# Performance work log

Measured on AMD Instinct MI355X. Metric: run time of the kernel, lower is better.

Reference implementation:

```python
import jax, jax.numpy as jnp
import numpy as np

B, D, T, NT, DS, G = 1024, 512, 36, 64, 32, 4
EPS = 1e-5


def setup_inputs() -> dict:
    key = jax.random.key(0)
    ks = jax.random.split(key, 8)
    return {
        "x": jax.random.normal(ks[0], (B, D, T, 1), jnp.float32),
        "y": jax.random.normal(ks[1], (B, D, T, 1), jnp.float32),
        "my_tokens": jax.random.normal(ks[2], (NT, D), jnp.float32) * 0.02,
        "gate": jax.random.normal(ks[3], (1,), jnp.float32) * 0.1,
        "gate_av": jax.random.normal(ks[4], (1,), jnp.float32) * 0.1,
        "w_down": jax.random.normal(ks[5], (DS, D // G), jnp.float32) * 0.05,  # Conv2d(512->32,1,groups=4) weight [32,128,1,1] squeezed
        "w_up": jax.random.normal(ks[6], (D, DS // G), jnp.float32) * 0.05,    # Conv2d(32->512,1,groups=4) weight [512,8,1,1] squeezed
        "bn1_g": jnp.ones((DS,), jnp.float32), "bn1_b": jnp.zeros((DS,), jnp.float32),
        "bn2_g": jnp.ones((D,), jnp.float32), "bn2_b": jnp.zeros((D,), jnp.float32),
        "lnb_g": jnp.ones((D,), jnp.float32), "lnb_b": jnp.zeros((D,), jnp.float32),
        "lnp_g": jnp.ones((D,), jnp.float32), "lnp_b": jnp.zeros((D,), jnp.float32),
    }


def _layernorm(h, g, b):  # normalize last dim
    mu = jnp.mean(h, axis=-1, keepdims=True)
    var = jnp.var(h, axis=-1, keepdims=True)
    return (h - mu) * jax.lax.rsqrt(var + EPS) * g + b


def _batchnorm(z, g, b):  # z: [B,C,T], training-mode batch stats over (B,T)
    mu = jnp.mean(z, axis=(0, 2), keepdims=True)
    var = jnp.var(z, axis=(0, 2), keepdims=True)
    return (z - mu) * jax.lax.rsqrt(var + EPS) * g[None, :, None] + b[None, :, None]


def reference(x, y, my_tokens, gate, gate_av, w_down, w_up,
              bn1_g, bn1_b, bn2_g, bn2_b, lnb_g, lnb_b, lnp_g, lnp_b):
    xs = x[..., 0]  # [B,D,T]
    ys = y[..., 0]  # [B,D,T]
    # token <- y cross attention
    att_y2tk = jax.nn.softmax(jnp.einsum('td,bds->bts', my_tokens, ys), axis=-1)  # [B,NT,T]
    rep = my_tokens[None] + jnp.einsum('bts,bds->btd', att_y2tk, ys)  # [B,NT,D]
    # x <- token cross attention
    att_tk2x = jax.nn.softmax(jnp.einsum('bds,btd->bst', xs, rep), axis=-1)  # [B,T,NT]
    x_res = jnp.einsum('bst,btd->bsd', att_tk2x, rep)  # [B,T,D]
    xc = xs + gate_av[0] * jnp.swapaxes(x_res, 1, 2)  # [B,D,T]
    # ln_before over channel dim
    h = jnp.swapaxes(_layernorm(jnp.swapaxes(xc, 1, 2), lnb_g, lnb_b), 1, 2)  # [B,D,T]
    # grouped 1x1 down conv
    hg = h.reshape(h.shape[0], G, D // G, T)
    z = jnp.einsum('bgct,goc->bgot', hg, w_down.reshape(G, DS // G, D // G)).reshape(h.shape[0], DS, T)
    z = jax.nn.relu(_batchnorm(z, bn1_g, bn1_b))
    # grouped 1x1 up conv
    zg = z.reshape(z.shape[0], G, DS // G, T)
    o = jnp.einsum('bgct,goc->bgot', zg, w_up.reshape(G, D // G, DS // G)).reshape(z.shape[0], D, T)
    o = _batchnorm(o, bn2_g, bn2_b)
    o = jnp.swapaxes(_layernorm(jnp.swapaxes(o, 1, 2), lnp_g, lnp_b), 1, 2)
    return (gate[0] * o)[..., None]  # [B,D,T,1]
```

## Files before the change

### kernel.cpp

```cpp
#include <hip/hip_runtime.h>

#define B_ 1024
#define D_ 512
#define T_ 36
#define NT_ 64
#define DS_ 32
#define EPS_ 1e-5f

typedef float f32x4 __attribute__((ext_vector_type(4)));
typedef __bf16 bf16x8 __attribute__((ext_vector_type(8)));
typedef unsigned short u16x8 __attribute__((ext_vector_type(8)));
typedef unsigned short u16x4 __attribute__((ext_vector_type(4)));

#define DEVI static __device__ __forceinline__
#define MFMA16 __builtin_amdgcn_mfma_f32_16x16x32_bf16

DEVI unsigned short f2bf(float f) { return __builtin_bit_cast(unsigned short, (__bf16)f); }
DEVI float bf2f(unsigned short h) { return (float)__builtin_bit_cast(__bf16, h); }

DEVI unsigned swz(int row, int col) {
    return (unsigned)(row * 1024 + ((2 * col) ^ ((row & 7) << 4)));
}

DEVI f32x4 tile16_gl(const unsigned short* __restrict__ Arow, const char* img, int brow, int l4)
{
    f32x4 acc0 = {0.f,0.f,0.f,0.f}, acc1 = {0.f,0.f,0.f,0.f};
    #pragma unroll
    for (int ks = 0; ks < 16; ks += 2) {
        int ka = ks * 32 + l4 * 8, kb = ka + 32;
        acc0 = MFMA16(*(const bf16x8*)(Arow + ka), *(const bf16x8*)(img + swz(brow, ka)), acc0, 0, 0, 0);
        acc1 = MFMA16(*(const bf16x8*)(Arow + kb), *(const bf16x8*)(img + swz(brow, kb)), acc1, 0, 0, 0);
    }
    return acc0 + acc1;
}

DEVI f32x4 tile16_ll(const char* imgA, int arow, const char* imgB, int brow, int l4)
{
    f32x4 acc0 = {0.f,0.f,0.f,0.f}, acc1 = {0.f,0.f,0.f,0.f};
    #pragma unroll
    for (int ks = 0; ks < 16; ks += 2) {
        int ka = ks * 32 + l4 * 8, kb = ka + 32;
        acc0 = MFMA16(*(const bf16x8*)(imgA + swz(arow, ka)), *(const bf16x8*)(imgB + swz(brow, ka)), acc0, 0, 0, 0);
        acc1 = MFMA16(*(const bf16x8*)(imgA + swz(arow, kb)), *(const bf16x8*)(imgB + swz(brow, kb)), acc1, 0, 0, 0);
    }
    return acc0 + acc1;
}

#define OFF_XST 49152
#define OFF_SC  98304
#define OFF_A1  109056
#define OFF_A1T 118272
#define OFF_A2  125184
#define OFF_GT  132096
#define OFF_W   139008
#define K1_LDS  145920

__global__ __launch_bounds__(512)
void k0_prepack(const float* __restrict__ tok, const float* __restrict__ wd,
                unsigned short* __restrict__ tokbf, unsigned short* __restrict__ tokT,
                unsigned short* __restrict__ wdd)
{
    int i = blockIdx.x * 512 + threadIdx.x;
    if (i < 32768) {
        tokbf[i] = f2bf(tok[i]);
    } else if (i < 65536) {
        int j = i - 32768; int d = j >> 6, t = j & 63;
        tokT[j] = f2bf(tok[t * 512 + d]);
    } else if (i < 81920) {
        int j = i - 65536; int o = j >> 9, dd = j & 511;
        wdd[j] = ((dd >> 7) == (o >> 3)) ? f2bf(wd[o * 128 + (dd & 127)]) : (unsigned short)0;
    }
}

DEVI void stage_unit(const float* __restrict__ src, char* __restrict__ dst, int u)
{
    int dblk = u / 9, s4 = u - dblk * 9;
    int s0 = s4 * 4;
    const float* bp = src + dblk * 8 * T_ + s0;
    u16x8 u0, u1, u2, u3;
    #pragma unroll
    for (int r = 0; r < 8; ++r) {
        f32x4 v = *(const f32x4*)(bp + r * T_);
        u0[r] = f2bf(v[0]); u1[r] = f2bf(v[1]);
        u2[r] = f2bf(v[2]); u3[r] = f2bf(v[3]);
    }
    *(u16x8*)(dst + swz(s0 + 0, dblk * 8)) = u0;
    *(u16x8*)(dst + swz(s0 + 1, dblk * 8)) = u1;
    *(u16x8*)(dst + swz(s0 + 2, dblk * 8)) = u2;
    *(u16x8*)(dst + swz(s0 + 3, dblk * 8)) = u3;
}

__global__ __launch_bounds__(1024, 4)
void k1_fused(const float* __restrict__ x, const float* __restrict__ y,
              const unsigned short* __restrict__ tokbf, const unsigned short* __restrict__ tokT,
              const float* __restrict__ gav_p, const unsigned short* __restrict__ wdd,
              const float* __restrict__ lnbg, const float* __restrict__ lnbb,
              float* __restrict__ z_pre)
{
    extern __shared__ char lds[];
    float* sc = (float*)(lds + OFF_SC);
    unsigned short* a1  = (unsigned short*)(lds + OFF_A1);
    unsigned short* a1t = (unsigned short*)(lds + OFF_A1T);
    unsigned short* a2  = (unsigned short*)(lds + OFF_A2);
    unsigned short* gt  = (unsigned short*)(lds + OFF_GT);
    unsigned short* wb  = (unsigned short*)(lds + OFF_W);

    const int b    = blockIdx.x;
    const int tid  = threadIdx.x;
    const int lane = tid & 63;
    const int w    = tid >> 6;
    const int l15  = lane & 15;
    const int l4   = lane >> 4;

    const float* yb = y + b * (D_ * T_);
    const float* xb = x + b * (D_ * T_);

    if (tid < 576) {
        stage_unit(yb, lds, tid);
    } else {
        int z = tid - 576;
        unsigned* z1 = (unsigned*)(lds + 36 * 1024);
        for (int i = z; i < 3072; i += 448) z1[i] = 0u;
        unsigned* z2 = (unsigned*)(lds + OFF_XST + 36 * 1024);
        for (int i = z; i < 3072; i += 448) z2[i] = 0u;
        unsigned* z3 = (unsigned*)(lds + OFF_A1);
        for (int i = z; i < 9216; i += 448) z3[i] = 0u;
    }
    __syncthreads();

    if (w < 12) {
        int mt = w / 3, nt = w % 3;
        int trow = mt * 16 + l15, srow = nt * 16 + l15;
        f32x4 acc = tile16_gl(tokbf + trow * 512, lds, srow, l4);
        if (srow < T_) {
            #pragma unroll
            for (int j = 0; j < 4; ++j)
                sc[(mt * 16 + l4 * 4 + j) * 42 + srow] = acc[j];
        }
    } else {
        for (int u = tid - 768; u < 576; u += 256)
            stage_unit(xb, lds + OFF_XST, u);
    }
    __syncthreads();

    if (w < 9) {
        int mt = w / 3, nt = w % 3;
        int arow = mt * 16 + l15, brow = nt * 16 + l15;
        f32x4 acc = tile16_ll(lds + OFF_XST, arow, lds, brow, l4);
        #pragma unroll
        for (int j = 0; j < 4; ++j) {
            int gr = mt * 16 + l4 * 4 + j;
            if (gr < T_) gt[gr * 72 + brow] = f2bf(acc[j]);
        }
    }
    __syncthreads();

    {
        int t = tid >> 4, l16 = tid & 15;
        const float* scp = sc + t * 42;
        float v0 = scp[l16];
        float v1 = scp[l16 + 16];
        float v2 = (l16 < 4) ? scp[l16 + 32] : -1e30f;
        float m = fmaxf(fmaxf(v0, v1), v2);
        #pragma unroll
        for (int off = 1; off < 16; off <<= 1) m = fmaxf(m, __shfl_xor(m, off));
        float e0 = __expf(v0 - m), e1 = __expf(v1 - m);
        float e2 = (l16 < 4) ? __expf(v2 - m) : 0.f;
        float ssum = e0 + e1 + e2;
        #pragma unroll
        for (int off = 1; off < 16; off <<= 1) ssum += __shfl_xor(ssum, off);
        float inv = 1.f / ssum;
        unsigned short h0 = f2bf(e0 * inv), h1 = f2bf(e1 * inv);
        a1[t * 72 + l16] = h0;       a1[t * 72 + l16 + 16] = h1;
        a1t[l16 * 72 + t] = h0;      a1t[(l16 + 16) * 72 + t] = h1;
        if (l16 < 4) {
            unsigned short h2 = f2bf(e2 * inv);
            a1[t * 72 + l16 + 32] = h2;
            a1t[(l16 + 32) * 72 + t] = h2;
        }
    }
    f32x4 py0[2], py1[2], py2[2];
    #pragma unroll
    for (int mi = 0; mi < 2; ++mi) {
        const float* yrow = yb + ((2 * w + mi) * 16 + l15) * T_;
        py0[mi] = *(const f32x4*)(yrow + l4 * 8);
        py1[mi] = *(const f32x4*)(yrow + l4 * 8 + 4);
        if (l4 == 0) py2[mi] = *(const f32x4*)(yrow + 32);
        else         py2[mi] = (f32x4){0.f, 0.f, 0.f, 0.f};
    }
    __syncthreads();

    if (w < 12) {
        int mt = w / 3, nt = w % 3;
        int trow = mt * 16 + l15, srow = nt * 16 + l15;
        bf16x8 sa0 = *(const bf16x8*)(a1 + trow * 72 + l4 * 8);
        bf16x8 sa1 = *(const bf16x8*)(a1 + trow * 72 + 32 + l4 * 8);
        bf16x8 sb0 = *(const bf16x8*)(gt + srow * 72 + l4 * 8);
        bf16x8 sb1 = *(const bf16x8*)(gt + srow * 72 + 32 + l4 * 8);
        f32x4 acc = tile16_gl(tokbf + trow * 512, lds + OFF_XST, srow, l4);
        acc = MFMA16(sa0, sb0, acc, 0, 0, 0);
        acc = MFMA16(sa1, sb1, acc, 0, 0, 0);
        if (srow < T_) {
            #pragma unroll
            for (int j = 0; j < 4; ++j)
                sc[(mt * 16 + l4 * 4 + j) * 42 + srow] = acc[j];
        }
    }
    __syncthreads();

    if (tid < 768) {
        int s = tid >> 4, l16 = tid & 15;
        if (s < T_) {
            float v0 = sc[(l16) * 42 + s];
            float v1 = sc[(l16 + 16) * 42 + s];
            float v2 = sc[(l16 + 32) * 42 + s];
            float v3 = sc[(l16 + 48) * 42 + s];
            float m = fmaxf(fmaxf(v0, v1), fmaxf(v2, v3));
            #pragma unroll
            for (int off = 1; off < 16; off <<= 1) m = fmaxf(m, __shfl_xor(m, off));
            float e0 = __expf(v0 - m), e1 = __expf(v1 - m), e2 = __expf(v2 - m), e3 = __expf(v3 - m);
            float ssum = e0 + e1 + e2 + e3;
            #pragma unroll
            for (int off = 1; off < 16; off <<= 1) ssum += __shfl_xor(ssum, off);
            float inv = 1.f / ssum;
            a2[s * 72 + l16]      = f2bf(e0 * inv);
            a2[s * 72 + l16 + 16] = f2bf(e1 * inv);
            a2[s * 72 + l16 + 32] = f2bf(e2 * inv);
            a2[s * 72 + l16 + 48] = f2bf(e3 * inv);
        }
    }
    __syncthreads();

    if (w < 9) {
        int mt = w / 3, nt = w % 3;
        f32x4 acc = {0.f, 0.f, 0.f, 0.f};
        #pragma unroll
        for (int ks = 0; ks < 2; ++ks) {
            int k0 = ks * 32 + l4 * 8;
            acc = MFMA16(*(const bf16x8*)(a2 + (mt * 16 + l15) * 72 + k0),
                         *(const bf16x8*)(a1t + (nt * 16 + l15) * 72 + k0), acc, 0, 0, 0);
        }
        #pragma unroll
        for (int j = 0; j < 4; ++j)
            wb[(mt * 16 + l4 * 4 + j) * 72 + nt * 16 + l15] = f2bf(acc[j]);
    }
    __syncthreads();

    {
        const float gav = gav_p[0];
        f32x4 acc[2][3];
        #pragma unroll
        for (int mi = 0; mi < 2; ++mi)
            #pragma unroll
            for (int n = 0; n < 3; ++n) acc[mi][n] = (f32x4){0.f, 0.f, 0.f, 0.f};

        bf16x8 aT[2][2], aY[2][2];
        #pragma unroll
        for (int mi = 0; mi < 2; ++mi) {
            int d = (2 * w + mi) * 16 + l15;
            aT[mi][0] = *(const bf16x8*)(tokT + d * 64 + l4 * 8);
            aT[mi][1] = *(const bf16x8*)(tokT + d * 64 + 32 + l4 * 8);
            bf16x8 t0, t1;
            #pragma unroll
            for (int j = 0; j < 4; ++j) {
                t0[j] = (__bf16)py0[mi][j]; t0[4 + j] = (__bf16)py1[mi][j];
                t1[j] = (__bf16)py2[mi][j]; t1[4 + j] = (__bf16)0.f;
            }
            aY[mi][0] = t0; aY[mi][1] = t1;
        }
        #pragma unroll
        for (int n = 0; n < 3; ++n) {
            int srow = n * 16 + l15;
            bf16x8 b20 = *(const bf16x8*)(a2 + srow * 72 + l4 * 8);
            bf16x8 b21 = *(const bf16x8*)(a2 + srow * 72 + 32 + l4 * 8);
            bf16x8 bw0 = *(const bf16x8*)(wb + srow * 72 + l4 * 8);
            bf16x8 bw1 = *(const bf16x8*)(wb + srow * 72 + 32 + l4 * 8);
            #pragma unroll
            for (int mi = 0; mi < 2; ++mi) {
                acc[mi][n] = MFMA16(aT[mi][0], b20, acc[mi][n], 0, 0, 0);
                acc[mi][n] = MFMA16(aT[mi][1], b21, acc[mi][n], 0, 0, 0);
                acc[mi][n] = MFMA16(aY[mi][0], bw0, acc[mi][n], 0, 0, 0);
                acc[mi][n] = MFMA16(aY[mi][1], bw1, acc[mi][n], 0, 0, 0);
            }
        }

        float* red = sc;
        float rs_[3] = {0.f, 0.f, 0.f}, rq_[3] = {0.f, 0.f, 0.f};
        #pragma unroll
        for (int mi = 0; mi < 2; ++mi) {
            int dcol = (2 * w + mi) * 16 + l4 * 4;
            #pragma unroll
            for (int n = 0; n < 3; ++n) {
                int s = n * 16 + l15;
                if (s < T_) {
                    u16x4 xv = *(const u16x4*)(lds + OFF_XST + swz(s, dcol));
                    #pragma unroll
                    for (int j = 0; j < 4; ++j) {
                        float v = bf2f(xv[j]) + gav * acc[mi][n][j];
                        acc[mi][n][j] = v;
                        rs_[n] += v; rq_[n] += v * v;
                    }
                }
            }
        }
        #pragma unroll
        for (int n = 0; n < 3; ++n) {
            rs_[n] += __shfl_xor(rs_[n], 16); rq_[n] += __shfl_xor(rq_[n], 16);
            rs_[n] += __shfl_xor(rs_[n], 32); rq_[n] += __shfl_xor(rq_[n], 32);
        }
        if (l4 == 0) {
            #pragma unroll
            for (int n = 0; n < 3; ++n) {
                int s = n * 16 + l15;
                if (s < T_) { red[s * 16 + w] = rs_[n]; red[768 + s * 16 + w] = rq_[n]; }
            }
        }
        __syncthreads();
        if (tid < T_) {
            int s = tid; float S = 0.f, Q = 0.f;
            #pragma unroll
            for (int q = 0; q < 16; ++q) { S += red[s * 16 + q]; Q += red[768 + s * 16 + q]; }
            float mu = S * (1.f / 512.f);
            float var = Q * (1.f / 512.f) - mu * mu;
            red[1536 + s] = mu; red[1584 + s] = rsqrtf(var + EPS_);
        }
        __syncthreads();

        #pragma unroll
        for (int mi = 0; mi < 2; ++mi) {
            int dcol = (2 * w + mi) * 16 + l4 * 4;
            f32x4 gv  = *(const f32x4*)(lnbg + dcol);
            f32x4 bv2 = *(const f32x4*)(lnbb + dcol);
            #pragma unroll
            for (int n = 0; n < 3; ++n) {
                int s = n * 16 + l15;
                if (s < T_) {
                    float mu = red[1536 + s], rsg = red[1584 + s];
                    u16x4 hv;
                    #pragma unroll
                    for (int j = 0; j < 4; ++j)
                        hv[j] = f2bf((acc[mi][n][j] - mu) * rsg * gv[j] + bv2[j]);
                    *(u16x4*)(lds + swz(s, dcol)) = hv;
                }
            }
        }
    }
    __syncthreads();

    if (w < 6) {
        int mt = w / 3, nt = w % 3;
        int orow = mt * 16 + l15, srow = nt * 16 + l15;
        f32x4 acc = tile16_gl(wdd + orow * 512, lds, srow, l4);
        if (srow < T_) {
            #pragma unroll
            for (int j = 0; j < 4; ++j)
                z_pre[b * (DS_ * T_) + (mt * 16 + l4 * 4 + j) * T_ + srow] = acc[j];
        }
    }
}

__global__ __launch_bounds__(256)
void k3_bn1(const float* __restrict__ z_pre, float* __restrict__ st1)
{
    __shared__ float rbuf[4][2];
    int o = blockIdx.x;
    int tid = threadIdx.x;
    float S = 0.f, Q = 0.f;
    for (int i = tid; i < B_ * T_; i += 256) {
        int b = i / T_, t = i - b * T_;
        float v = z_pre[b * (DS_ * T_) + o * T_ + t];
        S += v; Q += v * v;
    }
    #pragma unroll
    for (int off = 1; off < 64; off <<= 1) { S += __shfl_xor(S, off); Q += __shfl_xor(Q, off); }
    int ww = tid >> 6;
    if ((tid & 63) == 0) { rbuf[ww][0] = S; rbuf[ww][1] = Q; }
    __syncthreads();
    if (tid == 0) {
        float s2 = 0.f, q2 = 0.f;
        for (int i = 0; i < 4; ++i) { s2 += rbuf[i][0]; q2 += rbuf[i][1]; }
        float mu = s2 / 36864.f;
        float var = q2 / 36864.f - mu * mu;
        st1[o] = mu; st1[32 + o] = rsqrtf(var + EPS_);
    }
}

__global__ __launch_bounds__(256)
void k4m_moments(const float* __restrict__ z_pre, const float* __restrict__ st1,
                 const float* __restrict__ g1p, const float* __restrict__ b1p,
                 float* __restrict__ m4)
{
    __shared__ float zr[32][40];
    int blk = blockIdx.x, tid = threadIdx.x;
    int c2 = tid & 7, c1 = (tid >> 3) & 7, g = tid >> 6;
    int ch1 = g * 8 + c1, ch2 = g * 8 + c2;
    float acc = 0.f, asum = 0.f;
    for (int bi = 0; bi < 8; ++bi) {
        int b = blk * 8 + bi;
        __syncthreads();
        for (int i = tid; i < DS_ * T_; i += 256) {
            int o = i / T_, t = i - o * T_;
            float v = z_pre[b * (DS_ * T_) + i];
            zr[o][t] = fmaxf(0.f, (v - st1[o]) * st1[32 + o] * g1p[o] + b1p[o]);
        }
        __syncthreads();
        for (int t = 0; t < T_; ++t) {
            float a = zr[ch1][t], b2 = zr[ch2][t];
            acc += a * b2;
            asum += a;
        }
    }
    m4[blk * 288 + tid] = acc;
    if (c1 == c2) m4[blk * 288 + 256 + g * 8 + c1] = asum;
}

__global__ __launch_bounds__(512)
void k4s_bn2stats(const float* __restrict__ m4, const float* __restrict__ wu,
                  float* __restrict__ st2)
{
    __shared__ float M2[256], mz[32];
    int tid = threadIdx.x;
    if (tid < 256) {
        float S = 0.f;
        for (int k = 0; k < 128; ++k) S += m4[k * 288 + tid];
        M2[tid] = S * (1.f / 36864.f);
    } else if (tid < 288) {
        int j = tid - 256;
        float S = 0.f;
        for (int k = 0; k < 128; ++k) S += m4[k * 288 + 256 + j];
        mz[j] = S * (1.f / 36864.f);
    }
    __syncthreads();
    int d = tid, g = d >> 7;
    float wr[8];
    #pragma unroll
    for (int c = 0; c < 8; ++c) wr[c] = wu[d * 8 + c];
    float mu2 = 0.f;
    #pragma unroll
    for (int c = 0; c < 8; ++c) mu2 += wr[c] * mz[g * 8 + c];
    float e2 = 0.f;
    #pragma unroll
    for (int c = 0; c < 8; ++c)
        #pragma unroll
        for (int c2 = 0; c2 < 8; ++c2)
            e2 += wr[c] * wr[c2] * M2[g * 64 + c * 8 + c2];
    st2[d] = mu2;
    st2[512 + d] = rsqrtf(e2 - mu2 * mu2 + EPS_);
}

#define K5_LDS 47888
__global__ __launch_bounds__(512, 6)
void k5_final(const float* __restrict__ z_pre, const float* __restrict__ st1,
              const float* __restrict__ g1p, const float* __restrict__ b1p,
              const float* __restrict__ wu, const float* __restrict__ st2,
              const float* __restrict__ g2p, const float* __restrict__ b2p,
              const float* __restrict__ lnpg, const float* __restrict__ lnpb,
              const float* __restrict__ gate_p, float* __restrict__ out)
{
    extern __shared__ char lds[];
    unsigned short* o_f = (unsigned short*)lds;
    float* zrT = (float*)(lds + 41984);
    int b = blockIdx.x;
    int tid = threadIdx.x;

    for (int i = tid; i < DS_ * T_; i += 512) {
        int o = i / T_, s = i - o * T_;
        float v = z_pre[b * (DS_ * T_) + i];
        zrT[s * 41 + o] = fmaxf(0.f, (v - st1[o]) * st1[32 + o] * g1p[o] + b1p[o]);
    }
    __syncthreads();

    for (int i = tid; i < D_ * T_; i += 512) {
        int d = i / T_, t = i - d * T_;
        const float* zp = &zrT[t * 41 + (d >> 7) * 8];
        const float* wp = &wu[d * 8];
        f32x4 w0 = *(const f32x4*)wp;
        f32x4 w1 = *(const f32x4*)(wp + 4);
        float acc = zp[0]*w0[0] + zp[1]*w0[1] + zp[2]*w0[2] + zp[3]*w0[3]
                  + zp[4]*w1[0] + zp[5]*w1[1] + zp[6]*w1[2] + zp[7]*w1[3];
        o_f[d * 41 + t] = f2bf((acc - st2[d]) * st2[512 + d] * g2p[d] + b2p[d]);
    }
    __syncthreads();

    int w = tid >> 6, lane = tid & 63;
    float gate = gate_p[0];
    for (int t = w; t < T_; t += 8) {
        float S = 0.f, Q = 0.f;
        float v[8];
        #pragma unroll
        for (int i2 = 0; i2 < 8; ++i2) {
            float vv = bf2f(o_f[(i2 * 64 + lane) * 41 + t]);
            v[i2] = vv; S += vv; Q += vv * vv;
        }
        #pragma unroll
        for (int off = 1; off < 64; off <<= 1) { S += __shfl_xor(S, off); Q += __shfl_xor(Q, off); }
        float mu = S * (1.f / 512.f);
        float var = Q * (1.f / 512.f) - mu * mu;
        float rs = rsqrtf(var + EPS_);
        #pragma unroll
        for (int i2 = 0; i2 < 8; ++i2) {
            int d = i2 * 64 + lane;
            o_f[d * 41 + t] = f2bf(gate * ((v[i2] - mu) * rs * lnpg[d] + lnpb[d]));
        }
    }
    __syncthreads();

    float* ob = out + b * (D_ * T_);
    for (int i = tid; i < D_ * T_; i += 512) {
        int d = i / T_, t = i - d * T_;
        ob[i] = bf2f(o_f[d * 41 + t]);
    }
}

extern "C" void kernel_launch(void* const* d_in, const int* in_sizes, int n_in,
                              void* d_out, int out_size, void* d_ws, size_t ws_size,
                              hipStream_t stream)
{
    (void)in_sizes; (void)n_in; (void)out_size; (void)ws_size;
    const float* x    = (const float*)d_in[0];
    const float* y    = (const float*)d_in[1];
    const float* tok  = (const float*)d_in[2];
    const float* gate = (const float*)d_in[3];
    const float* gav  = (const float*)d_in[4];
    const float* wd   = (const float*)d_in[5];
    const float* wu   = (const float*)d_in[6];
    const float* bn1g = (const float*)d_in[7];
    const float* bn1b = (const float*)d_in[8];
    const float* bn2g = (const float*)d_in[9];
    const float* bn2b = (const float*)d_in[10];
    const float* lnbg = (const float*)d_in[11];
    const float* lnbb = (const float*)d_in[12];
    const float* lnpg = (const float*)d_in[13];
    const float* lnpb = (const float*)d_in[14];
    float* out = (float*)d_out;

    char* ws = (char*)d_ws;
    float* z_pre          = (float*)ws;
    float* st1            = (float*)(ws + 4718592);
    unsigned short* tokbf = (unsigned short*)(ws + 4719104);
    unsigned short* tokT  = (unsigned short*)(ws + 4784640);
    unsigned short* wdd   = (unsigned short*)(ws + 4850176);
    float* m4             = (float*)(ws + 4882944);
    float* st2            = (float*)(ws + 5030400);

    hipFuncSetAttribute((const void*)k1_fused, hipFuncAttributeMaxDynamicSharedMemorySize, K1_LDS);
    hipFuncSetAttribute((const void*)k5_final, hipFuncAttributeMaxDynamicSharedMemorySize, K5_LDS);

    k0_prepack<<<160, 512, 0, stream>>>(tok, wd, tokbf, tokT, wdd);
    k1_fused<<<B_, 1024, K1_LDS, stream>>>(x, y, tokbf, tokT, gav, wdd, lnbg, lnbb, z_pre);
    k3_bn1<<<DS_, 256, 0, stream>>>(z_pre, st1);
    k4m_moments<<<128, 256, 0, stream>>>(z_pre, st1, bn1g, bn1b, m4);
    k4s_bn2stats<<<1, 512, 0, stream>>>(m4, wu, st2);
    k5_final<<<B_, 512, K5_LDS, stream>>>(z_pre, st1, bn1g, bn1b, wu, st2, bn2g, bn2b,
                                          lnpg, lnpb, gate, out);
}
```

Before: 224.7 us.

## Split BN1 stats into 512-block partial reduction and move softmax to idle waves

The BN1 statistics kernel previously ran only 32 blocks, each striding over all 1024 batches. It is now split into a 512-block partial-sum pass and a small final reduction, so many more CUs share the reduction. In k1_fused, the first softmax moves off its own barrier phase onto waves 12-15, which were idle during the score GEMM, with each thread handling 9 elements. This removes one __syncthreads and overlaps the softmax with the tile GEMM, at the cost of one extra kernel launch and a workspace layout shift.

```diff
diff --git a/kernel.cpp b/kernel.cpp
--- a/kernel.cpp
+++ b/kernel.cpp
@@ -152,31 +152,27 @@
             int gr = mt * 16 + l4 * 4 + j;
             if (gr < T_) gt[gr * 72 + brow] = f2bf(acc[j]);
         }
-    }
-    __syncthreads();
-
-    {
-        int t = tid >> 4, l16 = tid & 15;
-        const float* scp = sc + t * 42;
-        float v0 = scp[l16];
-        float v1 = scp[l16 + 16];
-        float v2 = (l16 < 4) ? scp[l16 + 32] : -1e30f;
-        float m = fmaxf(fmaxf(v0, v1), v2);
-        #pragma unroll
-        for (int off = 1; off < 16; off <<= 1) m = fmaxf(m, __shfl_xor(m, off));
-        float e0 = __expf(v0 - m), e1 = __expf(v1 - m);
-        float e2 = (l16 < 4) ? __expf(v2 - m) : 0.f;
-        float ssum = e0 + e1 + e2;
-        #pragma unroll
-        for (int off = 1; off < 16; off <<= 1) ssum += __shfl_xor(ssum, off);
+    } else if (w >= 12) {
+        int t = (tid - 768) >> 2, l2 = tid & 3;
+        const float* scp = sc + t * 42 + l2 * 9;
+        float v[9];
+        float m = -1e30f;
+        #pragma unroll
+        for (int j = 0; j < 9; ++j) { v[j] = scp[j]; m = fmaxf(m, v[j]); }
+        m = fmaxf(m, __shfl_xor(m, 1));
+        m = fmaxf(m, __shfl_xor(m, 2));
+        float e[9], ssum = 0.f;
+        #pragma unroll
+        for (int j = 0; j < 9; ++j) { e[j] = __expf(v[j] - m); ssum += e[j]; }
+        ssum += __shfl_xor(ssum, 1);
+        ssum += __shfl_xor(ssum, 2);
         float inv = 1.f / ssum;
-        unsigned short h0 = f2bf(e0 * inv), h1 = f2bf(e1 * inv);
-        a1[t * 72 + l16] = h0;       a1[t * 72 + l16 + 16] = h1;
-        a1t[l16 * 72 + t] = h0;      a1t[(l16 + 16) * 72 + t] = h1;
-        if (l16 < 4) {
-            unsigned short h2 = f2bf(e2 * inv);
-            a1[t * 72 + l16 + 32] = h2;
-            a1t[(l16 + 32) * 72 + t] = h2;
+        #pragma unroll
+        for (int j = 0; j < 9; ++j) {
+            unsigned short h = f2bf(e[j] * inv);
+            int s = l2 * 9 + j;
+            a1[t * 72 + s] = h;
+            a1t[s * 72 + t] = h;
         }
     }
     f32x4 py0[2], py1[2], py2[2];
@@ -360,15 +356,16 @@
 }
 
 __global__ __launch_bounds__(256)
-void k3_bn1(const float* __restrict__ z_pre, float* __restrict__ st1)
+void k3a_bn1part(const float* __restrict__ z_pre, float* __restrict__ p3)
 {
     __shared__ float rbuf[4][2];
-    int o = blockIdx.x;
+    int blk = blockIdx.x;
+    int o = blk & 31, sl = blk >> 5;
     int tid = threadIdx.x;
     float S = 0.f, Q = 0.f;
-    for (int i = tid; i < B_ * T_; i += 256) {
-        int b = i / T_, t = i - b * T_;
-        float v = z_pre[b * (DS_ * T_) + o * T_ + t];
+    for (int i = tid; i < 64 * T_; i += 256) {
+        int bb = sl * 64 + i / T_, t = i - (i / T_) * T_;
+        float v = z_pre[bb * (DS_ * T_) + o * T_ + t];
         S += v; Q += v * v;
     }
     #pragma unroll
@@ -379,8 +376,22 @@
     if (tid == 0) {
         float s2 = 0.f, q2 = 0.f;
         for (int i = 0; i < 4; ++i) { s2 += rbuf[i][0]; q2 += rbuf[i][1]; }
-        float mu = s2 / 36864.f;
-        float var = q2 / 36864.f - mu * mu;
+        p3[blk * 2] = s2; p3[blk * 2 + 1] = q2;
+    }
+}
+
+__global__ __launch_bounds__(64)
+void k3b_bn1stats(const float* __restrict__ p3, float* __restrict__ st1)
+{
+    int o = threadIdx.x;
+    if (o < 32) {
+        float S = 0.f, Q = 0.f;
+        for (int sl = 0; sl < 16; ++sl) {
+            S += p3[((sl << 5) | o) * 2];
+            Q += p3[((sl << 5) | o) * 2 + 1];
+        }
+        float mu = S / 36864.f;
+        float var = Q / 36864.f - mu * mu;
         st1[o] = mu; st1[32 + o] = rsqrtf(var + EPS_);
     }
 }
@@ -540,15 +551,17 @@
     unsigned short* tokbf = (unsigned short*)(ws + 4719104);
     unsigned short* tokT  = (unsigned short*)(ws + 4784640);
     unsigned short* wdd   = (unsigned short*)(ws + 4850176);
-    float* m4             = (float*)(ws + 4882944);
-    float* st2            = (float*)(ws + 5030400);
+    float* p3             = (float*)(ws + 4882944);
+    float* m4             = (float*)(ws + 4887040);
+    float* st2            = (float*)(ws + 5034496);
 
     hipFuncSetAttribute((const void*)k1_fused, hipFuncAttributeMaxDynamicSharedMemorySize, K1_LDS);
     hipFuncSetAttribute((const void*)k5_final, hipFuncAttributeMaxDynamicSharedMemorySize, K5_LDS);
 
     k0_prepack<<<160, 512, 0, stream>>>(tok, wd, tokbf, tokT, wdd);
     k1_fused<<<B_, 1024, K1_LDS, stream>>>(x, y, tokbf, tokT, gav, wdd, lnbg, lnbb, z_pre);
-    k3_bn1<<<DS_, 256, 0, stream>>>(z_pre, st1);
+    k3a_bn1part<<<512, 256, 0, stream>>>(z_pre, p3);
+    k3b_bn1stats<<<1, 64, 0, stream>>>(p3, st1);
     k4m_moments<<<128, 256, 0, stream>>>(z_pre, st1, bn1g, bn1b, m4);
     k4s_bn2stats<<<1, 512, 0, stream>>>(m4, wu, st2);
     k5_final<<<B_, 512, K5_LDS, stream>>>(z_pre, st1, bn1g, bn1b, wu, st2, bn2g, bn2b,
```

New measurement: 183.0 us. -18.5%, faster.
